# Kernel optimization log

Measured on AMD Instinct MI355X. Metric: run time of the kernel, lower is better.

## Reference

```python
import jax, jax.numpy as jnp
import numpy as np

B, H, W, C = 32, 64, 64, 384
WS = 8            # window size (square)
NH = 12           # num heads
HD = C // NH      # head dim
SCALE = HD ** -0.5


def setup_inputs() -> dict:
    key = jax.random.key(0)
    ks = jax.random.split(key, 5)
    std = 0.02
    return {
        "x": jax.random.normal(ks[0], (B, H, W, C), dtype=jnp.float32),
        "w_qkv": jax.random.normal(ks[1], (C, 3 * C), dtype=jnp.float32) * std,
        "b_qkv": jnp.zeros((3 * C,), dtype=jnp.float32),
        "w_proj": jax.random.normal(ks[2], (C, C), dtype=jnp.float32) * std,
        "b_proj": jnp.zeros((C,), dtype=jnp.float32),
    }


def reference(x, w_qkv, b_qkv, w_proj, b_proj):
    b, h, w, c = x.shape
    nh_win, nw_win = h // WS, w // WS
    # window partition: (B, nh, WS, nw, WS, C) -> (B*nw_total, WS*WS, C)
    xw = x.reshape(b, nh_win, WS, nw_win, WS, c)
    xw = xw.transpose(0, 1, 3, 2, 4, 5).reshape(b * nh_win * nw_win, WS * WS, c)
    nW, T = xw.shape[0], WS * WS
    # qkv projection
    qkv = xw @ w_qkv + b_qkv                      # (nW, T, 3C)
    qkv = qkv.reshape(nW, T, 3, NH, HD).transpose(2, 0, 3, 1, 4)
    q, k, v = qkv[0], qkv[1], qkv[2]              # (nW, NH, T, HD)
    attn = jnp.einsum('wntd,wnsd->wnts', q, k) * SCALE
    attn = jax.nn.softmax(attn, axis=-1)
    out = jnp.einsum('wnts,wnsd->wntd', attn, v)  # (nW, NH, T, HD)
    out = out.transpose(0, 2, 1, 3).reshape(nW, T, c)
    out = out @ w_proj + b_proj
    # window reverse
    out = out.reshape(b, nh_win, nw_win, WS, WS, c)
    out = out.transpose(0, 1, 3, 2, 4, 5).reshape(b, h, w, c)
    return out
```

## Files before the change

### kernel.cpp

```cpp
#include <hip/hip_runtime.h>
#include <hip/hip_bf16.h>

typedef __bf16 bfv8 __attribute__((ext_vector_type(8)));
typedef float f32x4 __attribute__((ext_vector_type(4)));
typedef unsigned int u32;

#define MFMA(a,b,c) __builtin_amdgcn_mfma_f32_16x16x32_bf16((a),(b),(c),0,0,0)

constexpr int XW_LD = 392;

__global__ __launch_bounds__(256)
void prep_weights(const float* __restrict__ w_qkv, const float* __restrict__ w_proj,
                  unsigned short* __restrict__ qT, unsigned short* __restrict__ pT)
{
    int i = blockIdx.x * 256 + threadIdx.x;
    const int NQ = 1152 * 384;
    if (i < NQ) {
        int c = i / 384, k = i - c * 384;
        __bf16 h = (__bf16)w_qkv[k * 1152 + c];
        qT[i] = *(unsigned short*)&h;
    } else {
        int j = i - NQ;
        if (j < 384 * 384) {
            int c = j / 384, k = j - c * 384;
            __bf16 h = (__bf16)w_proj[k * 384 + c];
            pT[j] = *(unsigned short*)&h;
        }
    }
}

__device__ __forceinline__ u32 pkbf(float a, float b) {
    __bf16 x = (__bf16)a, y = (__bf16)b;
    unsigned short lo = *(unsigned short*)&x, hi = *(unsigned short*)&y;
    return ((u32)hi << 16) | lo;
}

__device__ __forceinline__ bfv8 conv_frag(u32 p00, u32 p01, u32 p10, u32 p11,
                                          int abase, bool selhi)
{
    union { u32 u[4]; bfv8 v; } cv;
    #pragma unroll
    for (int w = 0; w < 4; ++w) {
        const int addr = abase + (w >> 1) * 64;
        const int lo_ = __builtin_amdgcn_ds_bpermute(addr, (int)((w & 1) ? p01 : p00));
        const int hi_ = __builtin_amdgcn_ds_bpermute(addr, (int)((w & 1) ? p11 : p10));
        cv.u[w] = (u32)(selhi ? hi_ : lo_);
    }
    return cv.v;
}

__global__ __launch_bounds__(256, 3)
void win_attn(const float* __restrict__ x,
              const float* __restrict__ b_qkv,
              const float* __restrict__ b_proj,
              const unsigned short* __restrict__ qT_,
              const unsigned short* __restrict__ pT_,
              float* __restrict__ out)
{
    __shared__ __bf16 sX[64 * XW_LD];

    const __bf16* wqkvT  = (const __bf16*)qT_;
    const __bf16* wprojT = (const __bf16*)pT_;

    const int wid  = blockIdx.x;
    const int bb   = wid >> 6;
    const int wy   = (wid >> 3) & 7;
    const int wx   = wid & 7;
    const int tid  = threadIdx.x;
    const int lane = tid & 63;
    const int wv   = tid >> 6;
    const int lr   = lane & 15;
    const int lg   = lane >> 4;
    const int k8   = lg * 8;

    const size_t gbase = ((size_t)(bb * 64 + wy * 8) * 64 + wx * 8) * 384;

    {
        const float* xb = x + gbase;
        for (int i = tid; i < 64 * 96; i += 256) {
            int t  = i / 96;
            int c4 = (i - t * 96) * 4;
            const float4 v = *(const float4*)(xb + (size_t)((t >> 3) * 64 + (t & 7)) * 384 + c4);
            *(uint2*)&sX[t * XW_LD + c4] = make_uint2(pkbf(v.x, v.y), pkbf(v.z, v.w));
        }
    }
    __syncthreads();

    const int   abase = ((lg & 1) * 32 + lr) * 4;
    const bool  selhi = (lg & 2) != 0;
    const float SC    = 0.17677669529663687f;

    u32 opk[3][4][2][2];

    #pragma unroll 1
    for (int hl = 0; hl < 3; ++hl) {
        const int h  = wv * 3 + hl;
        const int cQ = h * 32, cK = cQ + 384, cV = cQ + 768;

        f32x4 aq[2][4], ak[2][4], av[4][2];
        #pragma unroll
        for (int a = 0; a < 2; ++a)
            #pragma unroll
            for (int b = 0; b < 4; ++b) { aq[a][b] = f32x4{0,0,0,0}; ak[a][b] = f32x4{0,0,0,0}; av[b][a] = f32x4{0,0,0,0}; }

        const __bf16* wqp = wqkvT + (size_t)(cQ + lr) * 384 + k8;
        const __bf16* wkp = wqkvT + (size_t)(cK + lr) * 384 + k8;
        const __bf16* wvp = wqkvT + (size_t)(cV + lr) * 384 + k8;
        const __bf16* xp  = &sX[lr * XW_LD + k8];

        __builtin_amdgcn_s_setprio(1);
        #pragma unroll 2
        for (int kk = 0; kk < 12; ++kk) {
            bfv8 xf[4], wqf[2], wkf[2], wvf[2];
            #pragma unroll
            for (int t4 = 0; t4 < 4; ++t4) xf[t4] = *(const bfv8*)(xp + t4 * 16 * XW_LD + kk * 32);
            #pragma unroll
            for (int hdt = 0; hdt < 2; ++hdt) {
                wqf[hdt] = *(const bfv8*)(wqp + (size_t)hdt * 16 * 384 + kk * 32);
                wkf[hdt] = *(const bfv8*)(wkp + (size_t)hdt * 16 * 384 + kk * 32);
                wvf[hdt] = *(const bfv8*)(wvp + (size_t)hdt * 16 * 384 + kk * 32);
            }
            #pragma unroll
            for (int hdt = 0; hdt < 2; ++hdt)
                #pragma unroll
                for (int t4 = 0; t4 < 4; ++t4) {
                    aq[hdt][t4] = MFMA(wqf[hdt], xf[t4], aq[hdt][t4]);
                    ak[hdt][t4] = MFMA(wkf[hdt], xf[t4], ak[hdt][t4]);
                    av[t4][hdt] = MFMA(xf[t4], wvf[hdt], av[t4][hdt]);
                }
        }
        __builtin_amdgcn_s_setprio(0);

        float bqv[2][4], bkv[2][4], bvv[2];
        #pragma unroll
        for (int hdt = 0; hdt < 2; ++hdt) {
            #pragma unroll
            for (int r = 0; r < 4; ++r) {
                bqv[hdt][r] = b_qkv[cQ + hdt * 16 + lg * 4 + r];
                bkv[hdt][r] = b_qkv[cK + hdt * 16 + lg * 4 + r];
            }
            bvv[hdt] = b_qkv[cV + hdt * 16 + lr];
        }

        u32 pkQ[2][4][2], pkK[2][4][2], pkV[4][2][2];
        #pragma unroll
        for (int hdt = 0; hdt < 2; ++hdt)
            #pragma unroll
            for (int t4 = 0; t4 < 4; ++t4)
                #pragma unroll
                for (int p = 0; p < 2; ++p) {
                    pkQ[hdt][t4][p] = pkbf((aq[hdt][t4][2 * p] + bqv[hdt][2 * p]) * SC,
                                           (aq[hdt][t4][2 * p + 1] + bqv[hdt][2 * p + 1]) * SC);
                    pkK[hdt][t4][p] = pkbf(ak[hdt][t4][2 * p] + bkv[hdt][2 * p],
                                           ak[hdt][t4][2 * p + 1] + bkv[hdt][2 * p + 1]);
                    pkV[t4][hdt][p] = pkbf(av[t4][hdt][2 * p] + bvv[hdt],
                                           av[t4][hdt][2 * p + 1] + bvv[hdt]);
                }

        bfv8 Qf[4];
        #pragma unroll
        for (int qt = 0; qt < 4; ++qt)
            Qf[qt] = conv_frag(pkQ[0][qt][0], pkQ[0][qt][1], pkQ[1][qt][0], pkQ[1][qt][1], abase, selhi);
        f32x4 st[4][4];
        __builtin_amdgcn_s_setprio(1);
        #pragma unroll
        for (int kt = 0; kt < 4; ++kt) {
            const bfv8 kf = conv_frag(pkK[0][kt][0], pkK[0][kt][1], pkK[1][kt][0], pkK[1][kt][1], abase, selhi);
            #pragma unroll
            for (int qt = 0; qt < 4; ++qt) {
                f32x4 z{};
                st[kt][qt] = MFMA(kf, Qf[qt], z);
            }
        }
        __builtin_amdgcn_s_setprio(0);

        float rinv[4];
        #pragma unroll
        for (int qt = 0; qt < 4; ++qt) {
            float mx = -1e30f;
            #pragma unroll
            for (int kt = 0; kt < 4; ++kt)
                #pragma unroll
                for (int r = 0; r < 4; ++r) mx = fmaxf(mx, st[kt][qt][r]);
            mx = fmaxf(mx, __shfl_xor(mx, 16, 64));
            mx = fmaxf(mx, __shfl_xor(mx, 32, 64));
            float sum = 0.f;
            #pragma unroll
            for (int kt = 0; kt < 4; ++kt)
                #pragma unroll
                for (int r = 0; r < 4; ++r) { st[kt][qt][r] = __expf(st[kt][qt][r] - mx); sum += st[kt][qt][r]; }
            sum += __shfl_xor(sum, 16, 64);
            sum += __shfl_xor(sum, 32, 64);
            rinv[qt] = 1.f / sum;
        }
        u32 pkP[4][4][2];
        #pragma unroll
        for (int qt = 0; qt < 4; ++qt)
            #pragma unroll
            for (int kt = 0; kt < 4; ++kt)
                #pragma unroll
                for (int p = 0; p < 2; ++p)
                    pkP[qt][kt][p] = pkbf(st[kt][qt][2 * p] * rinv[qt], st[kt][qt][2 * p + 1] * rinv[qt]);

        bfv8 Vf[2][2];
        #pragma unroll
        for (int ks = 0; ks < 2; ++ks)
            #pragma unroll
            for (int hdt = 0; hdt < 2; ++hdt)
                Vf[ks][hdt] = conv_frag(pkV[2 * ks][hdt][0], pkV[2 * ks][hdt][1],
                                        pkV[2 * ks + 1][hdt][0], pkV[2 * ks + 1][hdt][1], abase, selhi);
        f32x4 o[4][2];
        #pragma unroll
        for (int qt = 0; qt < 4; ++qt)
            #pragma unroll
            for (int hdt = 0; hdt < 2; ++hdt) o[qt][hdt] = f32x4{0,0,0,0};
        __builtin_amdgcn_s_setprio(1);
        #pragma unroll
        for (int qt = 0; qt < 4; ++qt)
            #pragma unroll
            for (int ks = 0; ks < 2; ++ks) {
                const bfv8 pf = conv_frag(pkP[qt][2 * ks][0], pkP[qt][2 * ks][1],
                                          pkP[qt][2 * ks + 1][0], pkP[qt][2 * ks + 1][1], abase, selhi);
                #pragma unroll
                for (int hdt = 0; hdt < 2; ++hdt)
                    o[qt][hdt] = MFMA(pf, Vf[ks][hdt], o[qt][hdt]);
            }
        __builtin_amdgcn_s_setprio(0);
        #pragma unroll
        for (int qt = 0; qt < 4; ++qt)
            #pragma unroll
            for (int hdt = 0; hdt < 2; ++hdt)
                #pragma unroll
                for (int p = 0; p < 2; ++p)
                    opk[hl][qt][hdt][p] = pkbf(o[qt][hdt][2 * p], o[qt][hdt][2 * p + 1]);
    }

    __syncthreads();

    #pragma unroll
    for (int hl = 0; hl < 3; ++hl)
        #pragma unroll
        for (int qt = 0; qt < 4; ++qt)
            #pragma unroll
            for (int hdt = 0; hdt < 2; ++hdt)
                #pragma unroll
                for (int p = 0; p < 2; ++p) {
                    const u32 u = opk[hl][qt][hdt][p];
                    const int row0 = qt * 16 + lg * 4 + 2 * p;
                    const int col  = (wv * 3 + hl) * 32 + hdt * 16 + lr;
                    unsigned short lo = (unsigned short)(u & 0xffff);
                    unsigned short hi = (unsigned short)(u >> 16);
                    sX[row0 * XW_LD + col]       = *(__bf16*)&lo;
                    sX[(row0 + 1) * XW_LD + col] = *(__bf16*)&hi;
                }
    __syncthreads();

    const int nb = wv * 96;
    f32x4 acc[4][6];
    {
        const __bf16* bp = wprojT + (size_t)(nb + lr) * 384 + k8;
        #pragma unroll
        for (int m = 0; m < 4; ++m)
            #pragma unroll
            for (int nt = 0; nt < 6; ++nt) acc[m][nt] = f32x4{0,0,0,0};
        __builtin_amdgcn_s_setprio(1);
        #pragma unroll 2
        for (int kk = 0; kk < 12; ++kk) {
            bfv8 bfr[6];
            #pragma unroll
            for (int nt = 0; nt < 6; ++nt)
                bfr[nt] = *(const bfv8*)(bp + (size_t)nt * 16 * 384 + kk * 32);
            #pragma unroll
            for (int m = 0; m < 4; ++m) {
                const bfv8 af = *(const bfv8*)&sX[(m * 16 + lr) * XW_LD + kk * 32 + k8];
                #pragma unroll
                for (int nt = 0; nt < 6; ++nt)
                    acc[m][nt] = MFMA(af, bfr[nt], acc[m][nt]);
            }
        }
        __builtin_amdgcn_s_setprio(0);
    }
    float bpj[6];
    #pragma unroll
    for (int nt = 0; nt < 6; ++nt) bpj[nt] = b_proj[nb + nt * 16 + lr];

    __syncthreads();
    float* sF = (float*)sX;
    float* ob = out + gbase;
    #pragma unroll
    for (int half = 0; half < 2; ++half) {
        #pragma unroll
        for (int mm = 0; mm < 2; ++mm) {
            const int m = half * 2 + mm;
            #pragma unroll
            for (int r = 0; r < 4; ++r) {
                const int row = mm * 16 + lg * 4 + r;
                #pragma unroll
                for (int nt = 0; nt < 6; ++nt)
                    sF[row * 384 + nb + nt * 16 + lr] = acc[m][nt][r] + bpj[nt];
            }
        }
        __syncthreads();
        for (int i = tid; i < 32 * 96; i += 256) {
            const int row = i / 96;
            const int c4  = (i - row * 96) * 4;
            const int t   = half * 32 + row;
            const float4 v = *(const float4*)&sF[row * 384 + c4];
            *(float4*)(ob + (size_t)((t >> 3) * 64 + (t & 7)) * 384 + c4) = v;
        }
        if (half == 0) __syncthreads();
    }
}

extern "C" void kernel_launch(void* const* d_in, const int* in_sizes, int n_in,
                              void* d_out, int out_size, void* d_ws, size_t ws_size,
                              hipStream_t stream)
{
    const float* x      = (const float*)d_in[0];
    const float* w_qkv  = (const float*)d_in[1];
    const float* b_qkv  = (const float*)d_in[2];
    const float* w_proj = (const float*)d_in[3];
    const float* b_proj = (const float*)d_in[4];
    float* out = (float*)d_out;

    unsigned short* qT = (unsigned short*)d_ws;
    unsigned short* pT = qT + 1152 * 384;

    const int NPREP = 1152 * 384 + 384 * 384;
    prep_weights<<<(NPREP + 255) / 256, 256, 0, stream>>>(w_qkv, w_proj, qT, pT);
    win_attn<<<2048, 256, 0, stream>>>(x, b_qkv, b_proj, qT, pT, out);
}
```

Baseline: 382.2 us.

## Double-buffer QKV and projection fragment loads; relax occupancy to two blocks

Software-pipelines the QKV and output-projection K loops with explicit A/B register buffers, so the global and LDS loads for the next K step are issued before the MFMAs of the current step. It also precomputes all P fragments via ds_bpermute before the PV MFMA loop. Launch bounds go from 3 to 2 blocks per CU, giving more registers to hold the extra buffers at the cost of less occupancy for latency hiding.

```diff
diff --git a/kernel.cpp b/kernel.cpp
--- a/kernel.cpp
+++ b/kernel.cpp
@@ -49,7 +49,7 @@
     return cv.v;
 }
 
-__global__ __launch_bounds__(256, 3)
+__global__ __launch_bounds__(256, 2)
 void win_attn(const float* __restrict__ x,
               const float* __restrict__ b_qkv,
               const float* __restrict__ b_proj,
@@ -108,28 +108,36 @@
         const __bf16* wvp = wqkvT + (size_t)(cV + lr) * 384 + k8;
         const __bf16* xp  = &sX[lr * XW_LD + k8];
 
-        __builtin_amdgcn_s_setprio(1);
-        #pragma unroll 2
-        for (int kk = 0; kk < 12; ++kk) {
-            bfv8 xf[4], wqf[2], wkf[2], wvf[2];
-            #pragma unroll
-            for (int t4 = 0; t4 < 4; ++t4) xf[t4] = *(const bfv8*)(xp + t4 * 16 * XW_LD + kk * 32);
-            #pragma unroll
-            for (int hdt = 0; hdt < 2; ++hdt) {
-                wqf[hdt] = *(const bfv8*)(wqp + (size_t)hdt * 16 * 384 + kk * 32);
-                wkf[hdt] = *(const bfv8*)(wkp + (size_t)hdt * 16 * 384 + kk * 32);
-                wvf[hdt] = *(const bfv8*)(wvp + (size_t)hdt * 16 * 384 + kk * 32);
-            }
-            #pragma unroll
-            for (int hdt = 0; hdt < 2; ++hdt)
-                #pragma unroll
-                for (int t4 = 0; t4 < 4; ++t4) {
-                    aq[hdt][t4] = MFMA(wqf[hdt], xf[t4], aq[hdt][t4]);
-                    ak[hdt][t4] = MFMA(wkf[hdt], xf[t4], ak[hdt][t4]);
-                    av[t4][hdt] = MFMA(xf[t4], wvf[hdt], av[t4][hdt]);
-                }
-        }
-        __builtin_amdgcn_s_setprio(0);
+        bfv8 xfA[4], wqA[2], wkA[2], wvA[2];
+        bfv8 xfB[4], wqB[2], wkB[2], wvB[2];
+
+#define LDQKV(XF, WQ, WK, WV, KK) do {                                                   \
+        _Pragma("unroll") for (int t4 = 0; t4 < 4; ++t4)                                 \
+            XF[t4] = *(const bfv8*)(xp + t4 * 16 * XW_LD + (KK) * 32);                   \
+        _Pragma("unroll") for (int hd = 0; hd < 2; ++hd) {                               \
+            WQ[hd] = *(const bfv8*)(wqp + (size_t)hd * 16 * 384 + (KK) * 32);            \
+            WK[hd] = *(const bfv8*)(wkp + (size_t)hd * 16 * 384 + (KK) * 32);            \
+            WV[hd] = *(const bfv8*)(wvp + (size_t)hd * 16 * 384 + (KK) * 32); } } while (0)
+
+#define FMQKV(XF, WQ, WK, WV) do {                                                       \
+        _Pragma("unroll") for (int hd = 0; hd < 2; ++hd)                                 \
+        _Pragma("unroll") for (int t4 = 0; t4 < 4; ++t4) {                               \
+            aq[hd][t4] = MFMA(WQ[hd], XF[t4], aq[hd][t4]);                               \
+            ak[hd][t4] = MFMA(WK[hd], XF[t4], ak[hd][t4]);                               \
+            av[t4][hd] = MFMA(XF[t4], WV[hd], av[t4][hd]); } } while (0)
+
+        LDQKV(xfA, wqA, wkA, wvA, 0);
+        #pragma unroll
+        for (int kp = 0; kp < 6; ++kp) {
+            LDQKV(xfB, wqB, wkB, wvB, 2 * kp + 1);
+            __builtin_amdgcn_s_setprio(1);
+            FMQKV(xfA, wqA, wkA, wvA);
+            __builtin_amdgcn_s_setprio(0);
+            if (kp < 5) LDQKV(xfA, wqA, wkA, wvA, 2 * kp + 2);
+            __builtin_amdgcn_s_setprio(1);
+            FMQKV(xfB, wqB, wkB, wvB);
+            __builtin_amdgcn_s_setprio(0);
+        }
 
         float bqv[2][4], bkv[2][4], bvv[2];
         #pragma unroll
@@ -209,6 +217,13 @@
             for (int hdt = 0; hdt < 2; ++hdt)
                 Vf[ks][hdt] = conv_frag(pkV[2 * ks][hdt][0], pkV[2 * ks][hdt][1],
                                         pkV[2 * ks + 1][hdt][0], pkV[2 * ks + 1][hdt][1], abase, selhi);
+        bfv8 Pf[4][2];
+        #pragma unroll
+        for (int qt = 0; qt < 4; ++qt)
+            #pragma unroll
+            for (int ks = 0; ks < 2; ++ks)
+                Pf[qt][ks] = conv_frag(pkP[qt][2 * ks][0], pkP[qt][2 * ks][1],
+                                       pkP[qt][2 * ks + 1][0], pkP[qt][2 * ks + 1][1], abase, selhi);
         f32x4 o[4][2];
         #pragma unroll
         for (int qt = 0; qt < 4; ++qt)
@@ -218,13 +233,10 @@
         #pragma unroll
         for (int qt = 0; qt < 4; ++qt)
             #pragma unroll
-            for (int ks = 0; ks < 2; ++ks) {
-                const bfv8 pf = conv_frag(pkP[qt][2 * ks][0], pkP[qt][2 * ks][1],
-                                          pkP[qt][2 * ks + 1][0], pkP[qt][2 * ks + 1][1], abase, selhi);
+            for (int ks = 0; ks < 2; ++ks)
                 #pragma unroll
                 for (int hdt = 0; hdt < 2; ++hdt)
-                    o[qt][hdt] = MFMA(pf, Vf[ks][hdt], o[qt][hdt]);
-            }
+                    o[qt][hdt] = MFMA(Pf[qt][ks], Vf[ks][hdt], o[qt][hdt]);
         __builtin_amdgcn_s_setprio(0);
         #pragma unroll
         for (int qt = 0; qt < 4; ++qt)
@@ -263,22 +275,32 @@
         for (int m = 0; m < 4; ++m)
             #pragma unroll
             for (int nt = 0; nt < 6; ++nt) acc[m][nt] = f32x4{0,0,0,0};
-        __builtin_amdgcn_s_setprio(1);
-        #pragma unroll 2
-        for (int kk = 0; kk < 12; ++kk) {
-            bfv8 bfr[6];
-            #pragma unroll
-            for (int nt = 0; nt < 6; ++nt)
-                bfr[nt] = *(const bfv8*)(bp + (size_t)nt * 16 * 384 + kk * 32);
-            #pragma unroll
-            for (int m = 0; m < 4; ++m) {
-                const bfv8 af = *(const bfv8*)&sX[(m * 16 + lr) * XW_LD + kk * 32 + k8];
-                #pragma unroll
-                for (int nt = 0; nt < 6; ++nt)
-                    acc[m][nt] = MFMA(af, bfr[nt], acc[m][nt]);
-            }
-        }
-        __builtin_amdgcn_s_setprio(0);
+
+        bfv8 bfA[6], afA[4], bfB[6], afB[4];
+
+#define LDPJ(BF, AF, KK) do {                                                            \
+        _Pragma("unroll") for (int nt = 0; nt < 6; ++nt)                                 \
+            BF[nt] = *(const bfv8*)(bp + (size_t)nt * 16 * 384 + (KK) * 32);             \
+        _Pragma("unroll") for (int m = 0; m < 4; ++m)                                    \
+            AF[m] = *(const bfv8*)&sX[(m * 16 + lr) * XW_LD + (KK) * 32 + k8]; } while (0)
+
+#define FMPJ(BF, AF) do {                                                                \
+        _Pragma("unroll") for (int m = 0; m < 4; ++m)                                    \
+        _Pragma("unroll") for (int nt = 0; nt < 6; ++nt)                                 \
+            acc[m][nt] = MFMA(AF[m], BF[nt], acc[m][nt]); } while (0)
+
+        LDPJ(bfA, afA, 0);
+        #pragma unroll
+        for (int kp = 0; kp < 6; ++kp) {
+            LDPJ(bfB, afB, 2 * kp + 1);
+            __builtin_amdgcn_s_setprio(1);
+            FMPJ(bfA, afA);
+            __builtin_amdgcn_s_setprio(0);
+            if (kp < 5) LDPJ(bfA, afA, 2 * kp + 2);
+            __builtin_amdgcn_s_setprio(1);
+            FMPJ(bfB, afB);
+            __builtin_amdgcn_s_setprio(0);
+        }
     }
     float bpj[6];
     #pragma unroll
```

After: 545.7 us. 42.8% more time.
